# Kernel optimization log

Measured on AMD Instinct MI355X. Metric: run time of the kernel, lower is better.

Reference implementation:

```python
import jax, jax.numpy as jnp
import numpy as np
from jax import lax

N_CLUSTERS = 9
N_ITER = 10
COMPACTNESS = 3.0
GRID = 24  # hard-coded 24x24 spatial grid in the source
EPS = 1e-8


def setup_inputs() -> dict:
    key = jax.random.key(0)
    image_emb = jax.random.normal(key, (128, GRID * GRID, 768), dtype=jnp.float32)
    return {"image_emb": image_emb}


def _augment(image_emb):
    # x varies along columns, y along rows (matches expand/.T in the torch code)
    x_pos = jnp.tile(jnp.arange(GRID, dtype=image_emb.dtype), GRID) * COMPACTNESS   # [576]
    y_pos = jnp.repeat(jnp.arange(GRID, dtype=image_emb.dtype), GRID) * COMPACTNESS # [576]
    B, P, _ = image_emb.shape
    sp = jnp.broadcast_to(jnp.stack([x_pos, y_pos], axis=-1), (B, P, 2))
    return jnp.concatenate([sp, image_emb], axis=2)  # [B, 576, D+2]


def _init_centroids(feats):
    # SSN-style init: average-pool the 24x24 grid into a 3x3 seed grid (9 clusters)
    B, P, C = feats.shape
    g = feats.reshape(B, 3, GRID // 3, 3, GRID // 3, C)
    return g.mean(axis=(2, 4)).reshape(B, N_CLUSTERS, C)  # [B, 9, C]


def _soft_assign(feats, centroids):
    # squared-distance via expansion; avoids [B,P,K,C] intermediate
    p2 = jnp.sum(feats * feats, axis=-1, keepdims=True)          # [B,P,1]
    c2 = jnp.sum(centroids * centroids, axis=-1)[:, None, :]     # [B,1,K]
    pc = jnp.einsum('bpc,bkc->bpk', feats, centroids)            # [B,P,K]
    dist = p2 - 2.0 * pc + c2
    return jax.nn.softmax(-dist, axis=2)                         # [B,P,K]


def reference(image_emb):
    feats = _augment(image_emb)            # [B, 576, D+2]
    init = _init_centroids(feats)          # [B, 9, D+2]

    def step(centroids, _):
        a = _soft_assign(feats, centroids)                       # [B,P,K]
        w = jnp.sum(a, axis=1)                                   # [B,K]
        new_c = jnp.einsum('bpk,bpc->bkc', a, feats) / (w[..., None] + EPS)
        return new_c, None

    centroids, _ = lax.scan(step, init, None, length=N_ITER)
    # final soft assignments (superpixel association map)
    return _soft_assign(feats, centroids)  # [B, 576, 9]
```

## Files before the change

kernel.cpp:

```cpp
#include <hip/hip_runtime.h>

#define NB 128
#define NP 576
#define NK 9
#define EMB 768
#define SGRID 24
#define COMPF 3.0f
#define NITER 10
#define EPSV 1e-8f
#define CSTR 772

typedef short v8s __attribute__((ext_vector_type(8)));
typedef float v4f __attribute__((ext_vector_type(4)));

__device__ __forceinline__ unsigned short f2b(float f) {
    unsigned x = __float_as_uint(f);
    unsigned r = (x + 0x7fffu + ((x >> 16) & 1u)) >> 16;
    return (unsigned short)r;
}
__device__ __forceinline__ float b2f(unsigned short u) {
    return __uint_as_float(((unsigned)u) << 16);
}

__device__ __forceinline__ void gload16(const unsigned short* g, unsigned short* l) {
    __builtin_amdgcn_global_load_lds(
        (const __attribute__((address_space(1))) unsigned int*)g,
        (__attribute__((address_space(3))) unsigned int*)l, 16, 0, 0);
}

__global__ __launch_bounds__(192) void init_k(const float* __restrict__ emb,
                                              unsigned short* __restrict__ embb,
                                              float* __restrict__ pcent,
                                              int* __restrict__ chgflag) {
    int blk = blockIdx.x, b = blk / 9, pb = blk % 9;
    int t = threadIdx.x;
    int ay = pb / 3;

    if (pb == 0 && t == 0) chgflag[b] = 0;

    float a0x=0,a0y=0,a0z=0,a0w=0, a1x=0,a1y=0,a1z=0,a1w=0, a2x=0,a2y=0,a2z=0,a2w=0;
    const float* eg = emb + ((size_t)b * NP + pb * 64) * EMB + t * 4;
    unsigned short* og = embb + ((size_t)b * NP + pb * 64) * EMB + t * 4;
    for (int p = 0; p < 64; ++p) {
        float4 f = *(const float4*)(eg + (size_t)p * EMB);
        ushort4 u;
        u.x = f2b(f.x); u.y = f2b(f.y); u.z = f2b(f.z); u.w = f2b(f.w);
        *(ushort4*)(og + (size_t)p * EMB) = u;
        int pg = pb * 64 + p;
        int sel = (pg % SGRID) >> 3;
        bool m0 = (sel == 0), m1 = (sel == 1), m2 = (sel == 2);
        a0x += m0 ? f.x : 0.f; a0y += m0 ? f.y : 0.f; a0z += m0 ? f.z : 0.f; a0w += m0 ? f.w : 0.f;
        a1x += m1 ? f.x : 0.f; a1y += m1 ? f.y : 0.f; a1z += m1 ? f.z : 0.f; a1w += m1 ? f.w : 0.f;
        a2x += m2 ? f.x : 0.f; a2y += m2 ? f.y : 0.f; a2z += m2 ? f.z : 0.f; a2w += m2 ? f.w : 0.f;
    }
    float* pc = pcent + (size_t)(b * 9 + pb) * NK * CSTR;
    #pragma unroll
    for (int k = 0; k < NK; ++k) {
        int s = k - ay * 3;
        float4 v = make_float4(0.f, 0.f, 0.f, 0.f);
        if (s == 0) v = make_float4(a0x, a0y, a0z, a0w);
        if (s == 1) v = make_float4(a1x, a1y, a1z, a1w);
        if (s == 2) v = make_float4(a2x, a2y, a2z, a2w);
        *(float4*)&pc[k * CSTR + t * 4] = v;
    }
    if (t < NK) {
        int s = t - ay * 3;
        float w = 0.f, sx = 0.f, sy = 0.f;
        if (s >= 0 && s < 3) {
            for (int p = 0; p < 64; ++p) {
                int pg = pb * 64 + p;
                if (((pg % SGRID) >> 3) == s) {
                    w += 1.f;
                    sx += (float)(pg % SGRID) * COMPF;
                    sy += (float)(pg / SGRID) * COMPF;
                }
            }
        }
        pc[t * CSTR + 768] = sx; pc[t * CSTR + 769] = sy; pc[t * CSTR + 770] = w;
    }
}

__global__ __launch_bounds__(256) void fused_k(
    const unsigned short* __restrict__ embb,
    const unsigned short* __restrict__ centb,
    const float* __restrict__ csp,
    float* __restrict__ pcent,
    unsigned char* __restrict__ prev,
    int* __restrict__ chgflag,
    int itFirst,
    float* __restrict__ out)
{
    __shared__ unsigned short sc[16][776];
    __shared__ __align__(16) unsigned short sa[4][3][16][64];
    __shared__ float scx[16], scy[16], sc2[16];
    __shared__ int swin[64];
    __shared__ int scnt[NK];
    __shared__ unsigned char splist[NK][64];
    __shared__ int tileChg;

    int blk = blockIdx.x;
    int b = blk / 9, pb = blk % 9;
    int t = threadIdx.x, lane = t & 63, wv = t >> 6;
    int r16 = lane & 15, g = lane >> 4;

    const unsigned short* cg = centb + (size_t)b * NK * EMB;
    for (int i = t; i < NK * 96; i += 256) {
        int k = i / 96, s = i % 96;
        *(v8s*)&sc[k][s * 8] = *(const v8s*)&cg[k * EMB + s * 8];
    }
    for (int i = t; i < 7 * 96; i += 256) {
        int k = 9 + i / 96, s = i % 96;
        v8s z = {0,0,0,0,0,0,0,0};
        *(v8s*)&sc[k][s * 8] = z;
    }
    if (t < 16) {
        scx[t] = (t < NK) ? csp[((size_t)b * NK + t) * 2 + 0] : 0.f;
        scy[t] = (t < NK) ? csp[((size_t)b * NK + t) * 2 + 1] : 0.f;
    }
    if (t == 0) tileChg = itFirst;

    const unsigned short* eg = embb + ((size_t)b * NP + pb * 64) * EMB;
    const unsigned short* gb = eg + (size_t)(wv * 16 + (lane >> 3)) * EMB
                                  + (size_t)(((lane & 7) ^ (lane >> 3)) * 8);

    gload16(gb,                 &sa[wv][0][0][0]);
    gload16(gb + 8 * EMB,       &sa[wv][0][8][0]);
    gload16(gb + 64,            &sa[wv][1][0][0]);
    gload16(gb + 8 * EMB + 64,  &sa[wv][1][8][0]);

    __syncthreads();

    for (int k = wv; k < NK; k += 4) {
        float s = 0.f;
        const unsigned short* ck = sc[k];
        #pragma unroll
        for (int c = 0; c < 12; ++c) { float v = b2f(ck[lane + c * 64]); s += v * v; }
        #pragma unroll
        for (int m = 1; m < 64; m <<= 1) s += __shfl_xor(s, m);
        if (lane == 0) sc2[k] = s + scx[k] * scx[k] + scy[k] * scy[k];
    }
    if (t >= NK && t < 16) sc2[t] = 1e30f;

    v4f acc = {0.f, 0.f, 0.f, 0.f};
    const unsigned short* scrow = sc[r16];
    int xk = r16 & 7;

    #pragma unroll
    for (int cn = 0; cn < 11; ++cn) {
        __builtin_amdgcn_sched_barrier(0);
        asm volatile("s_waitcnt vmcnt(2)" ::: "memory");
        __builtin_amdgcn_sched_barrier(0);
        if (cn < 10) {
            int sl = (cn + 2) % 3;
            gload16(gb + (cn + 2) * 64,           &sa[wv][sl][0][0]);
            gload16(gb + 8 * EMB + (cn + 2) * 64, &sa[wv][sl][8][0]);
        }
        int cur = cn % 3;
        v8s a0 = *(const v8s*)&sa[wv][cur][r16][((g) ^ xk) * 8];
        v8s b0 = *(const v8s*)&scrow[cn * 64 + g * 8];
        acc = __builtin_amdgcn_mfma_f32_16x16x32_bf16(a0, b0, acc, 0, 0, 0);
        v8s a1 = *(const v8s*)&sa[wv][cur][r16][((4 + g) ^ xk) * 8];
        v8s b1 = *(const v8s*)&scrow[cn * 64 + 32 + g * 8];
        acc = __builtin_amdgcn_mfma_f32_16x16x32_bf16(a1, b1, acc, 0, 0, 0);
    }
    __builtin_amdgcn_sched_barrier(0);
    asm volatile("s_waitcnt vmcnt(0)" ::: "memory");
    __builtin_amdgcn_sched_barrier(0);
    {
        v8s a0 = *(const v8s*)&sa[wv][2][r16][((g) ^ xk) * 8];
        v8s b0 = *(const v8s*)&scrow[11 * 64 + g * 8];
        acc = __builtin_amdgcn_mfma_f32_16x16x32_bf16(a0, b0, acc, 0, 0, 0);
        v8s a1 = *(const v8s*)&sa[wv][2][r16][((4 + g) ^ xk) * 8];
        v8s b1 = *(const v8s*)&scrow[11 * 64 + 32 + g * 8];
        acc = __builtin_amdgcn_mfma_f32_16x16x32_bf16(a1, b1, acc, 0, 0, 0);
    }

    __syncthreads();

    float cxv = scx[r16], cyv = scy[r16], c2v = sc2[r16];
    #pragma unroll
    for (int j = 0; j < 4; ++j) {
        int lr = wv * 16 + g * 4 + j;
        int p = pb * 64 + lr;
        float px = (float)(p % SGRID) * COMPF;
        float py = (float)(p / SGRID) * COMPF;
        float lg = 2.f * (acc[j] + px * cxv + py * cyv) - c2v;
        float mx = lg;
        mx = fmaxf(mx, __shfl_xor(mx, 1));
        mx = fmaxf(mx, __shfl_xor(mx, 2));
        mx = fmaxf(mx, __shfl_xor(mx, 4));
        mx = fmaxf(mx, __shfl_xor(mx, 8));
        if (!itFirst) {
            float e = __expf(lg - mx);
            float se = e;
            se += __shfl_xor(se, 1);
            se += __shfl_xor(se, 2);
            se += __shfl_xor(se, 4);
            se += __shfl_xor(se, 8);
            if (r16 < NK) out[((size_t)b * NP + p) * NK + r16] = e / se;
        }
        unsigned long long wm = __ballot(lg == mx);
        int ki = (int)(__ffsll((unsigned long long)((wm >> (lane & 48)) & 0xFFFFull)) - 1);
        if (r16 == 0) swin[lr] = ki;
    }
    __syncthreads();

    if (wv == 1) {
        unsigned char* prevb = prev + (size_t)b * NP + pb * 64;
        unsigned char neww = (unsigned char)swin[lane];
        if (!itFirst) {
            bool diff = (prevb[lane] != neww);
            unsigned long long dm = __ballot(diff);
            if (lane == 0 && dm != 0ull) { chgflag[b] = 1; tileChg = 1; }
        }
        prevb[lane] = neww;
    }
    {
        int myk = swin[lane];
        for (int kk = wv; kk < NK; kk += 4) {
            unsigned long long msk = __ballot(myk == kk);
            int pos = __popcll(msk & ((1ull << lane) - 1ull));
            if (myk == kk) splist[kk][pos] = (unsigned char)lane;
            if (lane == 0) scnt[kk] = __popcll(msk);
        }
    }
    __syncthreads();

    if (tileChg) {
        float* pc = pcent + (size_t)(b * 9 + pb) * NK * CSTR;
        if (t < NK) {
            int n = scnt[t];
            float sx = 0.f, sy = 0.f;
            for (int i = 0; i < n; ++i) {
                int p = pb * 64 + splist[t][i];
                sx += (float)(p % SGRID);
                sy += (float)(p / SGRID);
            }
            pc[t * CSTR + 768] = sx * COMPF;
            pc[t * CSTR + 769] = sy * COMPF;
            pc[t * CSTR + 770] = (float)n;
        }
        if (t < 192) {
            const unsigned short* e2 = eg + 4 * t;
            #pragma unroll
            for (int k = 0; k < NK; ++k) {
                int n = scnt[k];
                float a0 = 0.f, a1 = 0.f, a2 = 0.f, a3 = 0.f;
                for (int i = 0; i < n; ++i) {
                    int p = splist[k][i];
                    ushort4 u = *(const ushort4*)(e2 + (size_t)p * EMB);
                    a0 += b2f(u.x); a1 += b2f(u.y); a2 += b2f(u.z); a3 += b2f(u.w);
                }
                *(float4*)&pc[k * CSTR + t * 4] = make_float4(a0, a1, a2, a3);
            }
        }
    }
}

__global__ __launch_bounds__(256) void reduce_k(const float* __restrict__ pcent,
                                                unsigned short* __restrict__ centb,
                                                float* __restrict__ csp) {
    __shared__ float sw[NK];
    int b = blockIdx.x / 3, cb = blockIdx.x % 3;
    int t = threadIdx.x;
    const float* pc = pcent + (size_t)b * 9 * NK * CSTR;

    if (t < NK) {
        float w = 0.f, sx = 0.f, sy = 0.f;
        for (int s = 0; s < 9; ++s) {
            const float* q = pc + (size_t)(s * NK + t) * CSTR;
            sx += q[768]; sy += q[769]; w += q[770];
        }
        float wi = w + EPSV;
        sw[t] = wi;
        if (cb == 0) {
            csp[((size_t)b * NK + t) * 2 + 0] = sx / wi;
            csp[((size_t)b * NK + t) * 2 + 1] = sy / wi;
        }
    }
    __syncthreads();

    int c = cb * 256 + t;
    #pragma unroll
    for (int k = 0; k < NK; ++k) {
        float v = 0.f;
        #pragma unroll
        for (int s = 0; s < 9; ++s) v += pc[(size_t)(s * NK + k) * CSTR + c];
        centb[((size_t)b * NK + k) * EMB + c] = f2b(v / sw[k]);
    }
}

__global__ __launch_bounds__(576) void tail_k(
    const unsigned short* __restrict__ embb,
    const float* __restrict__ pcent,
    const unsigned char* __restrict__ prevg,
    const int* __restrict__ chgflag,
    float* __restrict__ out)
{
    __shared__ unsigned short sc[16][776];
    __shared__ unsigned short sa[3][2][48][64];
    __shared__ float cacc[NK][EMB];
    __shared__ float cw[NK], csx[NK], csy[NK];
    __shared__ float scx[16], scy[16], sc2[16];
    __shared__ unsigned char prev[NP];
    __shared__ unsigned char swin[3][48];
    __shared__ unsigned char splist[3][NK][48];
    __shared__ int scnt[3][NK];
    __shared__ int chg;

    int b = blockIdx.x;
    if (chgflag[b] == 0) return;

    int t = threadIdx.x, lane = t & 63, wv = t >> 6;
    int grp = wv / 3, wg = wv % 3, gt = t - grp * 192;
    int r16 = lane & 15, g = lane >> 4;
    const unsigned short* ib = embb + (size_t)b * NP * EMB;

    for (int i = t; i < 7 * 96; i += 576) {
        int k = 9 + i / 96, s = i % 96;
        v8s z = {0,0,0,0,0,0,0,0};
        *(v8s*)&sc[k][s * 8] = z;
    }
    if (t >= NK && t < 16) { scx[t] = 0.f; scy[t] = 0.f; sc2[t] = 1e30f; }
    for (int i = t; i < NP; i += 576) prev[i] = prevg[(size_t)b * NP + i];

    const float* pcb = pcent + (size_t)b * 9 * NK * CSTR;
    if (t < 192) {
        int ch = t * 4;
        #pragma unroll
        for (int k = 0; k < NK; ++k) {
            float4 s = make_float4(0.f, 0.f, 0.f, 0.f);
            #pragma unroll
            for (int s9 = 0; s9 < 9; ++s9) {
                float4 q = *(const float4*)&pcb[(size_t)(s9 * NK + k) * CSTR + ch];
                s.x += q.x; s.y += q.y; s.z += q.z; s.w += q.w;
            }
            cacc[k][ch] = s.x; cacc[k][ch+1] = s.y; cacc[k][ch+2] = s.z; cacc[k][ch+3] = s.w;
        }
    }
    if (t < NK) {
        float w = 0.f, sx = 0.f, sy = 0.f;
        for (int s9 = 0; s9 < 9; ++s9) {
            const float* q = pcb + (size_t)(s9 * NK + t) * CSTR;
            sx += q[768]; sy += q[769]; w += q[770];
        }
        cw[t] = w; csx[t] = sx; csy[t] = sy;
    }
    __syncthreads();

    for (int it = 2; it <= NITER; ++it) {
        bool lastPass = (it == NITER);

        if (t < 192) {
            int ch = t * 4;
            #pragma unroll
            for (int k = 0; k < NK; ++k) {
                float inv = 1.f / (cw[k] + EPSV);
                ushort4 u;
                u.x = f2b(cacc[k][ch] * inv);
                u.y = f2b(cacc[k][ch+1] * inv);
                u.z = f2b(cacc[k][ch+2] * inv);
                u.w = f2b(cacc[k][ch+3] * inv);
                *(ushort4*)&sc[k][ch] = u;
            }
        }
        if (t < NK) {
            float inv = 1.f / (cw[t] + EPSV);
            scx[t] = csx[t] * inv;
            scy[t] = csy[t] * inv;
        }
        __syncthreads();

        if (wv < NK) {
            float s = 0.f;
            const unsigned short* ck = sc[wv];
            #pragma unroll
            for (int c = 0; c < EMB / 64; ++c) {
                float v = b2f(ck[lane + c * 64]); s += v * v;
            }
            #pragma unroll
            for (int m = 1; m < 64; m <<= 1) s += __shfl_xor(s, m);
            if (lane == 0) sc2[wv] = s + scx[wv] * scx[wv] + scy[wv] * scy[wv];
        }
        for (int i = t; i < NK * EMB; i += 576) ((float*)cacc)[i] = 0.f;
        if (t < NK) { cw[t] = 0.f; csx[t] = 0.f; csy[t] = 0.f; }
        if (t == 0) chg = 0;
        __syncthreads();

        float acc2[NK][4];
        #pragma unroll
        for (int k = 0; k < NK; ++k) { acc2[k][0]=0.f; acc2[k][1]=0.f; acc2[k][2]=0.f; acc2[k][3]=0.f; }
        float wreg = 0.f, sxreg = 0.f, syreg = 0.f;

        for (int rd = 0; rd < 4; ++rd) {
            int tileBase = (rd * 3 + grp) * 48;
            int sr = gt >> 3, sl = gt & 7;
            int sphys = (sl ^ (sr & 7)) * 8;
            const unsigned short* gb = ib + (size_t)(tileBase + sr) * EMB + sl * 8;
            v8s s0 = *(const v8s*)(gb);
            v8s s1 = *(const v8s*)(gb + 24 * EMB);
            *(v8s*)&sa[grp][0][sr][sphys] = s0;
            *(v8s*)&sa[grp][0][sr + 24][sphys] = s1;

            v4f acc = {0.f, 0.f, 0.f, 0.f};
            int lrow = wg * 16 + r16;
            for (int cn = 0; cn < 12; ++cn) {
                v8s n0, n1;
                if (cn < 11) {
                    n0 = *(const v8s*)(gb + (cn + 1) * 64);
                    n1 = *(const v8s*)(gb + (cn + 1) * 64 + 24 * EMB);
                }
                __syncthreads();
                int cur = cn & 1;
                #pragma unroll
                for (int ks = 0; ks < 2; ++ks) {
                    v8s af = *(const v8s*)&sa[grp][cur][lrow][(((ks << 2) + g) ^ (r16 & 7)) << 3];
                    v8s bf = *(const v8s*)&sc[r16][cn * 64 + ks * 32 + g * 8];
                    acc = __builtin_amdgcn_mfma_f32_16x16x32_bf16(af, bf, acc, 0, 0, 0);
                }
                if (cn < 11) {
                    *(v8s*)&sa[grp][cur ^ 1][sr][sphys] = n0;
                    *(v8s*)&sa[grp][cur ^ 1][sr + 24][sphys] = n1;
                }
            }

            float cxv = scx[r16], cyv = scy[r16], c2v = sc2[r16];
            #pragma unroll
            for (int j = 0; j < 4; ++j) {
                int lr = wg * 16 + g * 4 + j;
                int p = tileBase + lr;
                float px = (float)(p % SGRID) * COMPF;
                float py = (float)(p / SGRID) * COMPF;
                float lg = 2.f * (acc[j] + px * cxv + py * cyv) - c2v;
                float mx = lg;
                mx = fmaxf(mx, __shfl_xor(mx, 1));
                mx = fmaxf(mx, __shfl_xor(mx, 2));
                mx = fmaxf(mx, __shfl_xor(mx, 4));
                mx = fmaxf(mx, __shfl_xor(mx, 8));
                float e = __expf(lg - mx);
                float se = e;
                se += __shfl_xor(se, 1);
                se += __shfl_xor(se, 2);
                se += __shfl_xor(se, 4);
                se += __shfl_xor(se, 8);
                if (r16 < NK) out[((size_t)b * NP + p) * NK + r16] = e / se;
                if (!lastPass) {
                    float m = lg; int ki = r16;
                    #pragma unroll
                    for (int d = 1; d < 16; d <<= 1) {
                        float om = __shfl_xor(m, d);
                        int oi = __shfl_xor(ki, d);
                        if (om > m || (om == m && oi < ki)) { m = om; ki = oi; }
                    }
                    if (r16 == 0) swin[grp][lr] = (unsigned char)ki;
                }
            }

            if (!lastPass) {
                __syncthreads();
                if (wg == 0) {
                    unsigned char myk = swin[grp][lane < 48 ? lane : 0];
                    bool diff = false;
                    if (lane < 48) {
                        int p = tileBase + lane;
                        diff = (prev[p] != myk);
                        prev[p] = myk;
                    }
                    unsigned long long dm = __ballot(diff);
                    if (lane == 0 && dm != 0ull) chg = 1;
                    unsigned long long lmask = (1ull << lane) - 1ull;
                    #pragma unroll
                    for (int kk = 0; kk < NK; ++kk) {
                        unsigned long long msk = __ballot(lane < 48 && myk == (unsigned char)kk);
                        int pos = __popcll(msk & lmask);
                        if (lane < 48 && myk == (unsigned char)kk)
                            splist[grp][kk][pos] = (unsigned char)lane;
                        if (lane == 0) scnt[grp][kk] = __popcll(msk);
                    }
                }
                __syncthreads();

                if (wg == 0 && lane < NK) {
                    int n = scnt[grp][lane];
                    float sx = 0.f, sy = 0.f;
                    for (int i = 0; i < n; ++i) {
                        int p = tileBase + splist[grp][lane][i];
                        sx += (float)(p % SGRID);
                        sy += (float)(p / SGRID);
                    }
                    wreg += (float)n; sxreg += sx; syreg += sy;
                }
                const unsigned short* e2 = ib + (size_t)tileBase * EMB + gt * 4;
                #pragma unroll
                for (int k = 0; k < NK; ++k) {
                    int n = scnt[grp][k];
                    float a0 = acc2[k][0], a1 = acc2[k][1], a2 = acc2[k][2], a3 = acc2[k][3];
                    for (int i = 0; i < n; ++i) {
                        int row = splist[grp][k][i];
                        ushort4 u = *(const ushort4*)(e2 + (size_t)row * EMB);
                        a0 += b2f(u.x); a1 += b2f(u.y); a2 += b2f(u.z); a3 += b2f(u.w);
                    }
                    acc2[k][0] = a0; acc2[k][1] = a1; acc2[k][2] = a2; acc2[k][3] = a3;
                }
            }
        }

        if (lastPass) break;
        if (chg == 0) break;

        for (int g3 = 0; g3 < 3; ++g3) {
            if (grp == g3) {
                int ch = gt * 4;
                #pragma unroll
                for (int k = 0; k < NK; ++k) {
                    cacc[k][ch]   += acc2[k][0];
                    cacc[k][ch+1] += acc2[k][1];
                    cacc[k][ch+2] += acc2[k][2];
                    cacc[k][ch+3] += acc2[k][3];
                }
                if (wg == 0 && lane < NK) {
                    cw[lane]  += wreg;
                    csx[lane] += sxreg * COMPF;
                    csy[lane] += syreg * COMPF;
                }
            }
            __syncthreads();
        }
    }
}

extern "C" void kernel_launch(void* const* d_in, const int* in_sizes, int n_in,
                              void* d_out, int out_size, void* d_ws, size_t ws_size,
                              hipStream_t stream) {
    const float* emb = (const float*)d_in[0];
    char* w = (char*)d_ws;
    unsigned short* embb = (unsigned short*)w;  w += (size_t)NB * NP * EMB * 2;
    float* pcent = (float*)w;                   w += (size_t)NB * 9 * NK * CSTR * 4;
    unsigned short* centb = (unsigned short*)w; w += (size_t)NB * NK * EMB * 2;
    float* csp = (float*)w;                     w += (size_t)NB * NK * 2 * 4;
    unsigned char* prev = (unsigned char*)w;    w += (size_t)NB * NP;
    int* chgflag = (int*)w;                     w += (size_t)NB * 4;

    init_k<<<NB * 9, 192, 0, stream>>>(emb, embb, pcent, chgflag);
    reduce_k<<<NB * 3, 256, 0, stream>>>(pcent, centb, csp);
    fused_k<<<NB * 9, 256, 0, stream>>>(embb, centb, csp, pcent, prev, chgflag, 1, (float*)d_out);
    reduce_k<<<NB * 3, 256, 0, stream>>>(pcent, centb, csp);
    fused_k<<<NB * 9, 256, 0, stream>>>(embb, centb, csp, pcent, prev, chgflag, 0, (float*)d_out);
    tail_k<<<NB, 576, 0, stream>>>(embb, pcent, prev, chgflag, (float*)d_out);
}
```

Baseline: 164.3 us.

## Retile fused kernel to 96 pixels per block with six waves

The fused assignment/accumulation kernel now covers 96 pixels per block with 384 threads (6 tiles per image instead of 9). Centroid LDS staging is reduced to 10 rows, with padding rows redirected to a single zero row. Winner compaction and the change check are restructured for 96 pixels. The partial-centroid reduction and tail kernel now read 6 partials. This cuts redundant centroid loads and partial-sum traffic, at the cost of fewer, larger blocks and a narrower per-thread centroid accumulation (2 channels instead of 4).

```diff
diff --git a/kernel.cpp b/kernel.cpp
--- a/kernel.cpp
+++ b/kernel.cpp
@@ -80,7 +80,7 @@
     }
 }
 
-__global__ __launch_bounds__(256) void fused_k(
+__global__ __launch_bounds__(384) void fused_k(
     const unsigned short* __restrict__ embb,
     const unsigned short* __restrict__ centb,
     const float* __restrict__ csp,
@@ -90,28 +90,27 @@
     int itFirst,
     float* __restrict__ out)
 {
-    __shared__ unsigned short sc[16][776];
-    __shared__ __align__(16) unsigned short sa[4][3][16][64];
+    __shared__ unsigned short sc[10][776];
+    __shared__ __align__(16) unsigned short sa[6][3][16][64];
     __shared__ float scx[16], scy[16], sc2[16];
-    __shared__ int swin[64];
+    __shared__ unsigned char swin[96];
     __shared__ int scnt[NK];
-    __shared__ unsigned char splist[NK][64];
+    __shared__ unsigned char splist[NK][96];
     __shared__ int tileChg;
 
     int blk = blockIdx.x;
-    int b = blk / 9, pb = blk % 9;
-    int t = threadIdx.x, lane = t & 63, wv = t >> 6;
+    int b = blk / 6, pb = blk % 6;
+    int t = threadIdx.x, lane = t & 63, wv = t / 64;
     int r16 = lane & 15, g = lane >> 4;
 
     const unsigned short* cg = centb + (size_t)b * NK * EMB;
-    for (int i = t; i < NK * 96; i += 256) {
+    for (int i = t; i < NK * 96; i += 384) {
         int k = i / 96, s = i % 96;
         *(v8s*)&sc[k][s * 8] = *(const v8s*)&cg[k * EMB + s * 8];
     }
-    for (int i = t; i < 7 * 96; i += 256) {
-        int k = 9 + i / 96, s = i % 96;
+    for (int i = t; i < 96; i += 384) {
         v8s z = {0,0,0,0,0,0,0,0};
-        *(v8s*)&sc[k][s * 8] = z;
+        *(v8s*)&sc[NK][i * 8] = z;
     }
     if (t < 16) {
         scx[t] = (t < NK) ? csp[((size_t)b * NK + t) * 2 + 0] : 0.f;
@@ -119,7 +118,7 @@
     }
     if (t == 0) tileChg = itFirst;
 
-    const unsigned short* eg = embb + ((size_t)b * NP + pb * 64) * EMB;
+    const unsigned short* eg = embb + ((size_t)b * NP + pb * 96) * EMB;
     const unsigned short* gb = eg + (size_t)(wv * 16 + (lane >> 3)) * EMB
                                   + (size_t)(((lane & 7) ^ (lane >> 3)) * 8);
 
@@ -130,7 +129,7 @@
 
     __syncthreads();
 
-    for (int k = wv; k < NK; k += 4) {
+    for (int k = wv; k < NK; k += 6) {
         float s = 0.f;
         const unsigned short* ck = sc[k];
         #pragma unroll
@@ -142,7 +141,7 @@
     if (t >= NK && t < 16) sc2[t] = 1e30f;
 
     v4f acc = {0.f, 0.f, 0.f, 0.f};
-    const unsigned short* scrow = sc[r16];
+    const unsigned short* scrow = sc[(r16 < NK) ? r16 : NK];
     int xk = r16 & 7;
 
     #pragma unroll
@@ -181,7 +180,7 @@
     #pragma unroll
     for (int j = 0; j < 4; ++j) {
         int lr = wv * 16 + g * 4 + j;
-        int p = pb * 64 + lr;
+        int p = pb * 96 + lr;
         float px = (float)(p % SGRID) * COMPF;
         float py = (float)(p / SGRID) * COMPF;
         float lg = 2.f * (acc[j] + px * cxv + py * cyv) - c2v;
@@ -201,27 +200,34 @@
         }
         unsigned long long wm = __ballot(lg == mx);
         int ki = (int)(__ffsll((unsigned long long)((wm >> (lane & 48)) & 0xFFFFull)) - 1);
-        if (r16 == 0) swin[lr] = ki;
+        if (r16 == 0) swin[lr] = (unsigned char)ki;
     }
     __syncthreads();
 
     if (wv == 1) {
-        unsigned char* prevb = prev + (size_t)b * NP + pb * 64;
-        unsigned char neww = (unsigned char)swin[lane];
-        if (!itFirst) {
-            bool diff = (prevb[lane] != neww);
-            unsigned long long dm = __ballot(diff);
-            if (lane == 0 && dm != 0ull) { chgflag[b] = 1; tileChg = 1; }
-        }
-        prevb[lane] = neww;
-    }
-    {
-        int myk = swin[lane];
-        for (int kk = wv; kk < NK; kk += 4) {
-            unsigned long long msk = __ballot(myk == kk);
-            int pos = __popcll(msk & ((1ull << lane) - 1ull));
-            if (myk == kk) splist[kk][pos] = (unsigned char)lane;
-            if (lane == 0) scnt[kk] = __popcll(msk);
+        unsigned char* prevb = prev + (size_t)b * NP + pb * 96;
+        unsigned char n0 = swin[lane < 48 ? lane : 0];
+        unsigned char n1 = swin[lane < 48 ? 48 + lane : 48];
+        bool d0 = false, d1 = false;
+        if (lane < 48) {
+            if (!itFirst) { d0 = (prevb[lane] != n0); d1 = (prevb[48 + lane] != n1); }
+            prevb[lane] = n0; prevb[48 + lane] = n1;
+        }
+        unsigned long long dm = __ballot(d0 || d1);
+        if (lane == 0 && !itFirst && dm != 0ull) { chgflag[b] = 1; tileChg = 1; }
+    }
+    if (wv == 0) {
+        int k0 = (lane < 48) ? (int)swin[lane] : 255;
+        int k1 = (lane < 48) ? (int)swin[48 + lane] : 255;
+        unsigned long long lmask = (1ull << lane) - 1ull;
+        #pragma unroll
+        for (int kk = 0; kk < NK; ++kk) {
+            unsigned long long m0 = __ballot(k0 == kk);
+            unsigned long long m1 = __ballot(k1 == kk);
+            int c0 = __popcll(m0);
+            if (k0 == kk) splist[kk][__popcll(m0 & lmask)] = (unsigned char)lane;
+            if (k1 == kk) splist[kk][c0 + __popcll(m1 & lmask)] = (unsigned char)(48 + lane);
+            if (lane == 0) scnt[kk] = c0 + __popcll(m1);
         }
     }
     __syncthreads();
@@ -232,34 +238,32 @@
             int n = scnt[t];
             float sx = 0.f, sy = 0.f;
             for (int i = 0; i < n; ++i) {
-                int p = pb * 64 + splist[t][i];
+                int p = pb * 96 + splist[t][i];
                 sx += (float)(p % SGRID);
                 sy += (float)(p / SGRID);
             }
             pc[t * CSTR + 768] = sx * COMPF;
             pc[t * CSTR + 769] = sy * COMPF;
-            pc[t * CSTR + 770] = (float)n;
-        }
-        if (t < 192) {
-            const unsigned short* e2 = eg + 4 * t;
-            #pragma unroll
-            for (int k = 0; k < NK; ++k) {
-                int n = scnt[k];
-                float a0 = 0.f, a1 = 0.f, a2 = 0.f, a3 = 0.f;
-                for (int i = 0; i < n; ++i) {
-                    int p = splist[k][i];
-                    ushort4 u = *(const ushort4*)(e2 + (size_t)p * EMB);
-                    a0 += b2f(u.x); a1 += b2f(u.y); a2 += b2f(u.z); a3 += b2f(u.w);
-                }
-                *(float4*)&pc[k * CSTR + t * 4] = make_float4(a0, a1, a2, a3);
-            }
+            pc[t * CSTR + 770] = (float)scnt[t];
+        }
+        const unsigned short* e2 = eg + 2 * t;
+        #pragma unroll
+        for (int k = 0; k < NK; ++k) {
+            int n = scnt[k];
+            float a0 = 0.f, a1 = 0.f;
+            for (int i = 0; i < n; ++i) {
+                int p = splist[k][i];
+                ushort2 u = *(const ushort2*)(e2 + (size_t)p * EMB);
+                a0 += b2f(u.x); a1 += b2f(u.y);
+            }
+            *(float2*)&pc[k * CSTR + 2 * t] = make_float2(a0, a1);
         }
     }
 }
 
 __global__ __launch_bounds__(256) void reduce_k(const float* __restrict__ pcent,
                                                 unsigned short* __restrict__ centb,
-                                                float* __restrict__ csp) {
+                                                float* __restrict__ csp, int nt) {
     __shared__ float sw[NK];
     int b = blockIdx.x / 3, cb = blockIdx.x % 3;
     int t = threadIdx.x;
@@ -267,7 +271,7 @@
 
     if (t < NK) {
         float w = 0.f, sx = 0.f, sy = 0.f;
-        for (int s = 0; s < 9; ++s) {
+        for (int s = 0; s < nt; ++s) {
             const float* q = pc + (size_t)(s * NK + t) * CSTR;
             sx += q[768]; sy += q[769]; w += q[770];
         }
@@ -284,8 +288,7 @@
     #pragma unroll
     for (int k = 0; k < NK; ++k) {
         float v = 0.f;
-        #pragma unroll
-        for (int s = 0; s < 9; ++s) v += pc[(size_t)(s * NK + k) * CSTR + c];
+        for (int s = 0; s < nt; ++s) v += pc[(size_t)(s * NK + k) * CSTR + c];
         centb[((size_t)b * NK + k) * EMB + c] = f2b(v / sw[k]);
     }
 }
@@ -331,7 +334,7 @@
         for (int k = 0; k < NK; ++k) {
             float4 s = make_float4(0.f, 0.f, 0.f, 0.f);
             #pragma unroll
-            for (int s9 = 0; s9 < 9; ++s9) {
+            for (int s9 = 0; s9 < 6; ++s9) {
                 float4 q = *(const float4*)&pcb[(size_t)(s9 * NK + k) * CSTR + ch];
                 s.x += q.x; s.y += q.y; s.z += q.z; s.w += q.w;
             }
@@ -340,7 +343,7 @@
     }
     if (t < NK) {
         float w = 0.f, sx = 0.f, sy = 0.f;
-        for (int s9 = 0; s9 < 9; ++s9) {
+        for (int s9 = 0; s9 < 6; ++s9) {
             const float* q = pcb + (size_t)(s9 * NK + t) * CSTR;
             sx += q[768]; sy += q[769]; w += q[770];
         }
@@ -542,9 +545,9 @@
     int* chgflag = (int*)w;                     w += (size_t)NB * 4;
 
     init_k<<<NB * 9, 192, 0, stream>>>(emb, embb, pcent, chgflag);
-    reduce_k<<<NB * 3, 256, 0, stream>>>(pcent, centb, csp);
-    fused_k<<<NB * 9, 256, 0, stream>>>(embb, centb, csp, pcent, prev, chgflag, 1, (float*)d_out);
-    reduce_k<<<NB * 3, 256, 0, stream>>>(pcent, centb, csp);
-    fused_k<<<NB * 9, 256, 0, stream>>>(embb, centb, csp, pcent, prev, chgflag, 0, (float*)d_out);
+    reduce_k<<<NB * 3, 256, 0, stream>>>(pcent, centb, csp, 9);
+    fused_k<<<NB * 6, 384, 0, stream>>>(embb, centb, csp, pcent, prev, chgflag, 1, (float*)d_out);
+    reduce_k<<<NB * 3, 256, 0, stream>>>(pcent, centb, csp, 6);
+    fused_k<<<NB * 6, 384, 0, stream>>>(embb, centb, csp, pcent, prev, chgflag, 0, (float*)d_out);
     tail_k<<<NB, 576, 0, stream>>>(embb, pcent, prev, chgflag, (float*)d_out);
 }
```

New measurement: 195.8 us. 19.2% more time.
